# Kernel optimization log

Hardware: AMD Instinct MI355X
Metric: run time of the kernel (lower is better)

The kernel has to match this reference:

```python
import jax, jax.numpy as jnp
import numpy as np

B, C, H, W = 16, 512, 48, 48


def setup_inputs() -> dict:
    key = jax.random.key(0)
    k1, k2 = jax.random.split(key)
    rgb = jax.random.normal(k1, (B, C, H, W), dtype=jnp.float32)
    depth = jax.random.normal(k2, (B, C, H, W), dtype=jnp.float32)
    return {"rgb": rgb, "depth": depth}


def reference(rgb, depth):
    b, c, h, w = rgb.shape
    hw = h * w
    q = rgb.reshape(b, c, hw)              # [B, C, HW]
    k = depth.reshape(b, c, hw)            # [B, C, HW]
    # channel-affinity: energy[b, i, j] = <rgb_chan_i, depth_chan_j>
    energy = jnp.einsum('bcn,bdn->bcd', q, k)   # [B, C, C]
    cl_index = jnp.argmax(energy, axis=2)       # [B, C] best-matching depth channel per rgb channel
    # gather matched depth channels and fuse
    gathered = depth[jnp.arange(b)[:, None], cl_index]  # [B, C, H, W]
    return rgb + gathered
```

## Files before the change

### kernel.cpp

```cpp
#include <hip/hip_runtime.h>
#include <stdint.h>

#define BATCH 16
#define CH    512
#define HW    2304
#define BM    128
#define BN    128
#define BK    32
#define NKT   (HW / BK)

typedef _Float16 half8  __attribute__((ext_vector_type(8)));
typedef float    f32x16 __attribute__((ext_vector_type(16)));

#define AH_OFF 0
#define AL_OFF 8192
#define BH_OFF 16384
#define BL_OFF 24576
#define BUF_SZ 32768

#define MFMA16 __builtin_amdgcn_mfma_f32_32x32x16_f16

__device__ __forceinline__ uint32_t f32_sortable(float f) {
    uint32_t u = __float_as_uint(f);
    return (u & 0x80000000u) ? ~u : (u | 0x80000000u);
}

__device__ __forceinline__ int swz(int r, int cb) {
    return r * 64 + (cb ^ ((r & 3) << 4));
}

__device__ __forceinline__ void cvt8(const float4& v0, const float4& v1,
                                     half8& h, half8& l) {
    float vv[8] = {v0.x, v0.y, v0.z, v0.w, v1.x, v1.y, v1.z, v1.w};
    #pragma unroll
    for (int j = 0; j < 8; ++j) {
        _Float16 hh = (_Float16)vv[j];
        h[j] = hh;
        l[j] = (_Float16)(vv[j] - (float)hh);
    }
}

__device__ __forceinline__ void load_tile(const float* aG, const float* bG, int k0,
                                          float4 (&av)[4], float4 (&bv)[4], int half) {
    av[0] = *(const float4*)(aG + k0 + half * 8 + 0);
    av[1] = *(const float4*)(aG + k0 + half * 8 + 4);
    av[2] = *(const float4*)(aG + k0 + half * 8 + 16);
    av[3] = *(const float4*)(aG + k0 + half * 8 + 20);
    bv[0] = *(const float4*)(bG + k0 + half * 8 + 0);
    bv[1] = *(const float4*)(bG + k0 + half * 8 + 4);
    bv[2] = *(const float4*)(bG + k0 + half * 8 + 16);
    bv[3] = *(const float4*)(bG + k0 + half * 8 + 20);
}

__device__ __forceinline__ void stage_tile(char* dst,
                                           const float4 (&av)[4], const float4 (&bv)[4],
                                           int row, int half) {
    half8 h, l;
    cvt8(av[0], av[1], h, l);
    *(half8*)(dst + AH_OFF + swz(row, half * 16)) = h;
    *(half8*)(dst + AL_OFF + swz(row, half * 16)) = l;
    cvt8(av[2], av[3], h, l);
    *(half8*)(dst + AH_OFF + swz(row, 32 + half * 16)) = h;
    *(half8*)(dst + AL_OFF + swz(row, 32 + half * 16)) = l;
    cvt8(bv[0], bv[1], h, l);
    *(half8*)(dst + BH_OFF + swz(row, half * 16)) = h;
    *(half8*)(dst + BL_OFF + swz(row, half * 16)) = l;
    cvt8(bv[2], bv[3], h, l);
    *(half8*)(dst + BH_OFF + swz(row, 32 + half * 16)) = h;
    *(half8*)(dst + BL_OFF + swz(row, 32 + half * 16)) = l;
}

__device__ __forceinline__ void compute_tile(const char* buf, int rA0, int rB0, int hb,
                                             f32x16& a00, f32x16& a01,
                                             f32x16& a10, f32x16& a11) {
    #pragma unroll
    for (int kc = 0; kc < 2; ++kc) {
        const int cb = kc * 32 + hb;
        half8 ah0 = *(const half8*)(buf + AH_OFF + swz(rA0,      cb));
        half8 ah1 = *(const half8*)(buf + AH_OFF + swz(rA0 + 32, cb));
        half8 al0 = *(const half8*)(buf + AL_OFF + swz(rA0,      cb));
        half8 al1 = *(const half8*)(buf + AL_OFF + swz(rA0 + 32, cb));
        half8 bh0 = *(const half8*)(buf + BH_OFF + swz(rB0,      cb));
        half8 bh1 = *(const half8*)(buf + BH_OFF + swz(rB0 + 32, cb));
        half8 bl0 = *(const half8*)(buf + BL_OFF + swz(rB0,      cb));
        half8 bl1 = *(const half8*)(buf + BL_OFF + swz(rB0 + 32, cb));
        a00 = MFMA16(ah0, bh0, a00, 0, 0, 0);
        a01 = MFMA16(ah0, bh1, a01, 0, 0, 0);
        a10 = MFMA16(ah1, bh0, a10, 0, 0, 0);
        a11 = MFMA16(ah1, bh1, a11, 0, 0, 0);
        a00 = MFMA16(ah0, bl0, a00, 0, 0, 0);
        a01 = MFMA16(ah0, bl1, a01, 0, 0, 0);
        a10 = MFMA16(ah1, bl0, a10, 0, 0, 0);
        a11 = MFMA16(ah1, bl1, a11, 0, 0, 0);
        a00 = MFMA16(al0, bh0, a00, 0, 0, 0);
        a01 = MFMA16(al0, bh1, a01, 0, 0, 0);
        a10 = MFMA16(al1, bh0, a10, 0, 0, 0);
        a11 = MFMA16(al1, bh1, a11, 0, 0, 0);
    }
}

__global__ __launch_bounds__(256, 1)
void energy_argmax_kernel(const float* __restrict__ q,
                          const float* __restrict__ kmat,
                          unsigned long long* __restrict__ best)
{
    const int bid = blockIdx.x;
    const int nid = (bid & 7) * 32 + (bid >> 3);
    const int d0  = (nid & 3) * BN;
    const int c0  = ((nid >> 2) & 3) * BM;
    const int b   = nid >> 4;

    const int tid = threadIdx.x;
    const int lane = tid & 63;
    const int w    = tid >> 6;
    const int wm   = w >> 1;
    const int wn   = w & 1;

    __shared__ __align__(16) char sm[2 * BUF_SZ];
    char* buf0 = sm;
    char* buf1 = sm + BUF_SZ;

    const float* qb = q    + (size_t)b * CH * HW;
    const float* kb = kmat + (size_t)b * CH * HW;

    const int row  = tid >> 1, half = tid & 1;
    const float* aG = qb + (size_t)(c0 + row) * HW;
    const float* bG = kb + (size_t)(d0 + row) * HW;

    float4 av0[4], bv0[4], av1[4], bv1[4];

    load_tile(aG, bG, 0, av0, bv0, half);
    stage_tile(buf0, av0, bv0, row, half);
    load_tile(aG, bG, BK, av1, bv1, half);
    __syncthreads();

    f32x16 a00 = {}, a01 = {}, a10 = {}, a11 = {};

    const int rA0 = wm * 64 + (lane & 31);
    const int rB0 = wn * 64 + (lane & 31);
    const int hb  = (lane >> 5) * 16;

    for (int kt = 0; kt < NKT; kt += 2) {
        if (kt + 2 < NKT) load_tile(aG, bG, (kt + 2) * BK, av0, bv0, half);
        compute_tile(buf0, rA0, rB0, hb, a00, a01, a10, a11);
        stage_tile(buf1, av1, bv1, row, half);
        __syncthreads();
        if (kt + 3 < NKT) load_tile(aG, bG, (kt + 3) * BK, av1, bv1, half);
        compute_tile(buf1, rA0, rB0, hb, a00, a01, a10, a11);
        if (kt + 2 < NKT) stage_tile(buf0, av0, bv0, row, half);
        __syncthreads();
    }

    const uint32_t didx0 = ~(uint32_t)(d0 + wn * 64 +      (lane & 31));
    const uint32_t didx1 = ~(uint32_t)(d0 + wn * 64 + 32 + (lane & 31));
    #pragma unroll
    for (int mi = 0; mi < 2; ++mi) {
        #pragma unroll
        for (int qr = 0; qr < 16; ++qr) {
            float v0 = (mi == 0) ? a00[qr] : a10[qr];
            float v1 = (mi == 0) ? a01[qr] : a11[qr];
            int rowl = wm * 64 + mi * 32 + (qr & 3) + 8 * (qr >> 2) + 4 * (lane >> 5);
            unsigned long long p0 =
                ((unsigned long long)f32_sortable(v0) << 32) | didx0;
            unsigned long long p1 =
                ((unsigned long long)f32_sortable(v1) << 32) | didx1;
            unsigned long long p = p0 > p1 ? p0 : p1;
            #pragma unroll
            for (int off = 1; off < 32; off <<= 1) {
                unsigned long long o = __shfl_xor(p, off, 64);
                if (o > p) p = o;
            }
            if ((lane & 31) == 0)
                atomicMax(&best[(size_t)b * CH + c0 + rowl], p);
        }
    }
}

__global__ __launch_bounds__(256)
void gather_add_kernel(const float* __restrict__ rgb,
                       const float* __restrict__ depth,
                       const unsigned long long* __restrict__ best,
                       float* __restrict__ out)
{
    const int row = blockIdx.x;
    const int b   = row >> 9;
    const uint32_t idx = ~(uint32_t)(best[row] & 0xFFFFFFFFull);
    const float4* src = (const float4*)(rgb   + (size_t)row * HW);
    const float4* dep = (const float4*)(depth + ((size_t)b * CH + idx) * HW);
    float4*       dst = (float4*)(out + (size_t)row * HW);
    for (int j = threadIdx.x; j < HW / 4; j += 256) {
        float4 a = src[j], d = dep[j];
        float4 r; r.x = a.x + d.x; r.y = a.y + d.y; r.z = a.z + d.z; r.w = a.w + d.w;
        dst[j] = r;
    }
}

extern "C" void kernel_launch(void* const* d_in, const int* in_sizes, int n_in,
                              void* d_out, int out_size, void* d_ws, size_t ws_size,
                              hipStream_t stream)
{
    const float* rgb   = (const float*)d_in[0];
    const float* depth = (const float*)d_in[1];
    float* out = (float*)d_out;
    unsigned long long* best = (unsigned long long*)d_ws;

    hipMemsetAsync(best, 0, (size_t)BATCH * CH * sizeof(unsigned long long), stream);

    energy_argmax_kernel<<<256, 256, 0, stream>>>(rgb, depth, best);

    gather_add_kernel<<<BATCH * CH, 256, 0, stream>>>(rgb, depth, best, out);
}
```

Before: 126.9 us.

## Stream fp32 tiles via direct-to-LDS DMA with triple buffering and split-K warps

Replaces the register-staged global loads and per-tile fp16 hi/lo conversion with global_load_lds DMA of raw fp32 tiles into a swizzled, triple-buffered LDS ring. The hi/lo split now happens at fragment read time. Block size doubles to 512 threads so two warp groups each handle half of every K tile, and their partial accumulators are reduced through LDS before the argmax. This aims to remove VGPR staging and conversion work from the load path and overlap memory with MFMA. The cost is redundant conversion per fragment read, more LDS (96KB), and an extra reduction step.

```diff
diff --git a/kernel.cpp b/kernel.cpp
--- a/kernel.cpp
+++ b/kernel.cpp
@@ -12,10 +12,7 @@
 typedef _Float16 half8  __attribute__((ext_vector_type(8)));
 typedef float    f32x16 __attribute__((ext_vector_type(16)));
 
-#define AH_OFF 0
-#define AL_OFF 8192
-#define BH_OFF 16384
-#define BL_OFF 24576
+#define TILE_A 16384
 #define BUF_SZ 32768
 
 #define MFMA16 __builtin_amdgcn_mfma_f32_32x32x16_f16
@@ -25,12 +22,29 @@
     return (u & 0x80000000u) ? ~u : (u | 0x80000000u);
 }
 
-__device__ __forceinline__ int swz(int r, int cb) {
-    return r * 64 + (cb ^ ((r & 3) << 4));
-}
-
-__device__ __forceinline__ void cvt8(const float4& v0, const float4& v1,
-                                     half8& h, half8& l) {
+__device__ __forceinline__ int swzf32(int r, int s) {
+    return r * 128 + ((s ^ (r & 7)) << 4);
+}
+
+__device__ __forceinline__ void dma16(const float* g, char* l) {
+    __builtin_amdgcn_global_load_lds(
+        (const __attribute__((address_space(1))) void*)g,
+        (__attribute__((address_space(3))) void*)l, 16, 0, 0);
+}
+
+__device__ __forceinline__ void dma_step(char* lb, const float* gA0, const float* gA1,
+                                         const float* gB0, const float* gB1,
+                                         int ko, int w2) {
+    dma16(gA0 + ko, lb + w2 * 1024);
+    dma16(gA1 + ko, lb + w2 * 1024 + 1024);
+    dma16(gB0 + ko, lb + TILE_A + w2 * 1024);
+    dma16(gB1 + ko, lb + TILE_A + w2 * 1024 + 1024);
+}
+
+__device__ __forceinline__ void rdfrag(const char* base, int r, int s0,
+                                       half8& h, half8& l) {
+    float4 v0 = *(const float4*)(base + swzf32(r, s0));
+    float4 v1 = *(const float4*)(base + swzf32(r, s0 + 1));
     float vv[8] = {v0.x, v0.y, v0.z, v0.w, v1.x, v1.y, v1.z, v1.w};
     #pragma unroll
     for (int j = 0; j < 8; ++j) {
@@ -40,66 +54,46 @@
     }
 }
 
-__device__ __forceinline__ void load_tile(const float* aG, const float* bG, int k0,
-                                          float4 (&av)[4], float4 (&bv)[4], int half) {
-    av[0] = *(const float4*)(aG + k0 + half * 8 + 0);
-    av[1] = *(const float4*)(aG + k0 + half * 8 + 4);
-    av[2] = *(const float4*)(aG + k0 + half * 8 + 16);
-    av[3] = *(const float4*)(aG + k0 + half * 8 + 20);
-    bv[0] = *(const float4*)(bG + k0 + half * 8 + 0);
-    bv[1] = *(const float4*)(bG + k0 + half * 8 + 4);
-    bv[2] = *(const float4*)(bG + k0 + half * 8 + 16);
-    bv[3] = *(const float4*)(bG + k0 + half * 8 + 20);
-}
-
-__device__ __forceinline__ void stage_tile(char* dst,
-                                           const float4 (&av)[4], const float4 (&bv)[4],
-                                           int row, int half) {
-    half8 h, l;
-    cvt8(av[0], av[1], h, l);
-    *(half8*)(dst + AH_OFF + swz(row, half * 16)) = h;
-    *(half8*)(dst + AL_OFF + swz(row, half * 16)) = l;
-    cvt8(av[2], av[3], h, l);
-    *(half8*)(dst + AH_OFF + swz(row, 32 + half * 16)) = h;
-    *(half8*)(dst + AL_OFF + swz(row, 32 + half * 16)) = l;
-    cvt8(bv[0], bv[1], h, l);
-    *(half8*)(dst + BH_OFF + swz(row, half * 16)) = h;
-    *(half8*)(dst + BL_OFF + swz(row, half * 16)) = l;
-    cvt8(bv[2], bv[3], h, l);
-    *(half8*)(dst + BH_OFF + swz(row, 32 + half * 16)) = h;
-    *(half8*)(dst + BL_OFF + swz(row, 32 + half * 16)) = l;
-}
-
-__device__ __forceinline__ void compute_tile(const char* buf, int rA0, int rB0, int hb,
+__device__ __forceinline__ void compute_step(const char* buf, int rA0, int rB0, int s0,
                                              f32x16& a00, f32x16& a01,
                                              f32x16& a10, f32x16& a11) {
-    #pragma unroll
-    for (int kc = 0; kc < 2; ++kc) {
-        const int cb = kc * 32 + hb;
-        half8 ah0 = *(const half8*)(buf + AH_OFF + swz(rA0,      cb));
-        half8 ah1 = *(const half8*)(buf + AH_OFF + swz(rA0 + 32, cb));
-        half8 al0 = *(const half8*)(buf + AL_OFF + swz(rA0,      cb));
-        half8 al1 = *(const half8*)(buf + AL_OFF + swz(rA0 + 32, cb));
-        half8 bh0 = *(const half8*)(buf + BH_OFF + swz(rB0,      cb));
-        half8 bh1 = *(const half8*)(buf + BH_OFF + swz(rB0 + 32, cb));
-        half8 bl0 = *(const half8*)(buf + BL_OFF + swz(rB0,      cb));
-        half8 bl1 = *(const half8*)(buf + BL_OFF + swz(rB0 + 32, cb));
-        a00 = MFMA16(ah0, bh0, a00, 0, 0, 0);
-        a01 = MFMA16(ah0, bh1, a01, 0, 0, 0);
-        a10 = MFMA16(ah1, bh0, a10, 0, 0, 0);
-        a11 = MFMA16(ah1, bh1, a11, 0, 0, 0);
-        a00 = MFMA16(ah0, bl0, a00, 0, 0, 0);
-        a01 = MFMA16(ah0, bl1, a01, 0, 0, 0);
-        a10 = MFMA16(ah1, bl0, a10, 0, 0, 0);
-        a11 = MFMA16(ah1, bl1, a11, 0, 0, 0);
-        a00 = MFMA16(al0, bh0, a00, 0, 0, 0);
-        a01 = MFMA16(al0, bh1, a01, 0, 0, 0);
-        a10 = MFMA16(al1, bh0, a10, 0, 0, 0);
-        a11 = MFMA16(al1, bh1, a11, 0, 0, 0);
-    }
-}
-
-__global__ __launch_bounds__(256, 1)
+    const char* bA = buf;
+    const char* bB = buf + TILE_A;
+    half8 ah0, al0, ah1, al1, bh0, bl0, bh1, bl1;
+    rdfrag(bA, rA0,      s0, ah0, al0);
+    rdfrag(bA, rA0 + 32, s0, ah1, al1);
+    rdfrag(bB, rB0,      s0, bh0, bl0);
+    rdfrag(bB, rB0 + 32, s0, bh1, bl1);
+    a00 = MFMA16(ah0, bh0, a00, 0, 0, 0);
+    a01 = MFMA16(ah0, bh1, a01, 0, 0, 0);
+    a10 = MFMA16(ah1, bh0, a10, 0, 0, 0);
+    a11 = MFMA16(ah1, bh1, a11, 0, 0, 0);
+    a00 = MFMA16(ah0, bl0, a00, 0, 0, 0);
+    a01 = MFMA16(ah0, bl1, a01, 0, 0, 0);
+    a10 = MFMA16(ah1, bl0, a10, 0, 0, 0);
+    a11 = MFMA16(ah1, bl1, a11, 0, 0, 0);
+    a00 = MFMA16(al0, bh0, a00, 0, 0, 0);
+    a01 = MFMA16(al0, bh1, a01, 0, 0, 0);
+    a10 = MFMA16(al1, bh0, a10, 0, 0, 0);
+    a11 = MFMA16(al1, bh1, a11, 0, 0, 0);
+}
+
+#define STACC(A, aidx) { \
+    char* bp = sm + (p * 4 + (aidx)) * 4096 + lane * 64; \
+    *(float4*)(bp + ((0 ^ (lane & 3)) << 4)) = make_float4(A[0], A[1], A[2], A[3]); \
+    *(float4*)(bp + ((1 ^ (lane & 3)) << 4)) = make_float4(A[4], A[5], A[6], A[7]); \
+    *(float4*)(bp + ((2 ^ (lane & 3)) << 4)) = make_float4(A[8], A[9], A[10], A[11]); \
+    *(float4*)(bp + ((3 ^ (lane & 3)) << 4)) = make_float4(A[12], A[13], A[14], A[15]); }
+
+#define LDACC(A, aidx) { \
+    const char* bp = sm + (p * 4 + (aidx)) * 4096 + lane * 64; \
+    float4 v; \
+    v = *(const float4*)(bp + ((0 ^ (lane & 3)) << 4)); A[0]+=v.x; A[1]+=v.y; A[2]+=v.z; A[3]+=v.w; \
+    v = *(const float4*)(bp + ((1 ^ (lane & 3)) << 4)); A[4]+=v.x; A[5]+=v.y; A[6]+=v.z; A[7]+=v.w; \
+    v = *(const float4*)(bp + ((2 ^ (lane & 3)) << 4)); A[8]+=v.x; A[9]+=v.y; A[10]+=v.z; A[11]+=v.w; \
+    v = *(const float4*)(bp + ((3 ^ (lane & 3)) << 4)); A[12]+=v.x; A[13]+=v.y; A[14]+=v.z; A[15]+=v.w; }
+
+__global__ __launch_bounds__(512, 2)
 void energy_argmax_kernel(const float* __restrict__ q,
                           const float* __restrict__ kmat,
                           unsigned long long* __restrict__ best)
@@ -110,68 +104,76 @@
     const int c0  = ((nid >> 2) & 3) * BM;
     const int b   = nid >> 4;
 
-    const int tid = threadIdx.x;
+    const int tid  = threadIdx.x;
     const int lane = tid & 63;
     const int w    = tid >> 6;
-    const int wm   = w >> 1;
-    const int wn   = w & 1;
-
-    __shared__ __align__(16) char sm[2 * BUF_SZ];
-    char* buf0 = sm;
-    char* buf1 = sm + BUF_SZ;
+    const int kc   = w >> 2;
+    const int p    = w & 3;
+    const int wm   = p >> 1, wn = p & 1;
+    const int w2   = 2 * w;
+
+    __shared__ __align__(16) char sm[3 * BUF_SZ];
 
     const float* qb = q    + (size_t)b * CH * HW;
     const float* kb = kmat + (size_t)b * CH * HW;
 
-    const int row  = tid >> 1, half = tid & 1;
-    const float* aG = qb + (size_t)(c0 + row) * HW;
-    const float* bG = kb + (size_t)(d0 + row) * HW;
-
-    float4 av0[4], bv0[4], av1[4], bv1[4];
-
-    load_tile(aG, bG, 0, av0, bv0, half);
-    stage_tile(buf0, av0, bv0, row, half);
-    load_tile(aG, bG, BK, av1, bv1, half);
-    __syncthreads();
+    const int dml = (lane >> 3) * HW + (((lane & 7) ^ (lane >> 3)) << 2);
+    const float* gA0 = qb + (size_t)(c0 + 16 * w)     * HW + dml;
+    const float* gA1 = qb + (size_t)(c0 + 16 * w + 8) * HW + dml;
+    const float* gB0 = kb + (size_t)(d0 + 16 * w)     * HW + dml;
+    const float* gB1 = kb + (size_t)(d0 + 16 * w + 8) * HW + dml;
+
+    dma_step(sm,          gA0, gA1, gB0, gB1, 0,  w2);
+    dma_step(sm + BUF_SZ, gA0, gA1, gB0, gB1, BK, w2);
+    asm volatile("s_waitcnt vmcnt(4)" ::: "memory");
+    __builtin_amdgcn_s_barrier();
+    __builtin_amdgcn_sched_barrier(0);
 
     f32x16 a00 = {}, a01 = {}, a10 = {}, a11 = {};
-
     const int rA0 = wm * 64 + (lane & 31);
     const int rB0 = wn * 64 + (lane & 31);
-    const int hb  = (lane >> 5) * 16;
-
-    for (int kt = 0; kt < NKT; kt += 2) {
-        if (kt + 2 < NKT) load_tile(aG, bG, (kt + 2) * BK, av0, bv0, half);
-        compute_tile(buf0, rA0, rB0, hb, a00, a01, a10, a11);
-        stage_tile(buf1, av1, bv1, row, half);
-        __syncthreads();
-        if (kt + 3 < NKT) load_tile(aG, bG, (kt + 3) * BK, av1, bv1, half);
-        compute_tile(buf1, rA0, rB0, hb, a00, a01, a10, a11);
-        if (kt + 2 < NKT) stage_tile(buf0, av0, bv0, row, half);
-        __syncthreads();
-    }
-
-    const uint32_t didx0 = ~(uint32_t)(d0 + wn * 64 +      (lane & 31));
-    const uint32_t didx1 = ~(uint32_t)(d0 + wn * 64 + 32 + (lane & 31));
-    #pragma unroll
-    for (int mi = 0; mi < 2; ++mi) {
+    const int s0  = 4 * kc + 2 * (lane >> 5);
+
+    for (int t = 0; t < NKT - 2; ++t) {
+        dma_step(sm + ((t + 2) % 3) * BUF_SZ, gA0, gA1, gB0, gB1, (t + 2) * BK, w2);
+        compute_step(sm + (t % 3) * BUF_SZ, rA0, rB0, s0, a00, a01, a10, a11);
+        asm volatile("s_waitcnt vmcnt(4)" ::: "memory");
+        __builtin_amdgcn_s_barrier();
+        __builtin_amdgcn_sched_barrier(0);
+    }
+    compute_step(sm + ((NKT - 2) % 3) * BUF_SZ, rA0, rB0, s0, a00, a01, a10, a11);
+    asm volatile("s_waitcnt vmcnt(0)" ::: "memory");
+    __builtin_amdgcn_s_barrier();
+    __builtin_amdgcn_sched_barrier(0);
+    compute_step(sm + ((NKT - 1) % 3) * BUF_SZ, rA0, rB0, s0, a00, a01, a10, a11);
+
+    if (w >= 4) { STACC(a00, 0) STACC(a01, 1) STACC(a10, 2) STACC(a11, 3) }
+    __syncthreads();
+    if (w < 4) {
+        LDACC(a00, 0) LDACC(a01, 1) LDACC(a10, 2) LDACC(a11, 3)
+
+        const uint32_t didx0 = ~(uint32_t)(d0 + wn * 64 +      (lane & 31));
+        const uint32_t didx1 = ~(uint32_t)(d0 + wn * 64 + 32 + (lane & 31));
         #pragma unroll
-        for (int qr = 0; qr < 16; ++qr) {
-            float v0 = (mi == 0) ? a00[qr] : a10[qr];
-            float v1 = (mi == 0) ? a01[qr] : a11[qr];
-            int rowl = wm * 64 + mi * 32 + (qr & 3) + 8 * (qr >> 2) + 4 * (lane >> 5);
-            unsigned long long p0 =
-                ((unsigned long long)f32_sortable(v0) << 32) | didx0;
-            unsigned long long p1 =
-                ((unsigned long long)f32_sortable(v1) << 32) | didx1;
-            unsigned long long p = p0 > p1 ? p0 : p1;
+        for (int mi = 0; mi < 2; ++mi) {
             #pragma unroll
-            for (int off = 1; off < 32; off <<= 1) {
-                unsigned long long o = __shfl_xor(p, off, 64);
-                if (o > p) p = o;
+            for (int qr = 0; qr < 16; ++qr) {
+                float v0 = (mi == 0) ? a00[qr] : a10[qr];
+                float v1 = (mi == 0) ? a01[qr] : a11[qr];
+                int rowl = wm * 64 + mi * 32 + (qr & 3) + 8 * (qr >> 2) + 4 * (lane >> 5);
+                unsigned long long p0 =
+                    ((unsigned long long)f32_sortable(v0) << 32) | didx0;
+                unsigned long long p1 =
+                    ((unsigned long long)f32_sortable(v1) << 32) | didx1;
+                unsigned long long pk = p0 > p1 ? p0 : p1;
+                #pragma unroll
+                for (int off = 1; off < 32; off <<= 1) {
+                    unsigned long long o = __shfl_xor(pk, off, 64);
+                    if (o > pk) pk = o;
+                }
+                if ((lane & 31) == 0)
+                    atomicMax(&best[(size_t)b * CH + c0 + rowl], pk);
             }
-            if ((lane & 31) == 0)
-                atomicMax(&best[(size_t)b * CH + c0 + rowl], p);
         }
     }
 }
@@ -206,7 +208,7 @@
 
     hipMemsetAsync(best, 0, (size_t)BATCH * CH * sizeof(unsigned long long), stream);
 
-    energy_argmax_kernel<<<256, 256, 0, stream>>>(rgb, depth, best);
+    energy_argmax_kernel<<<256, 512, 0, stream>>>(rgb, depth, best);
 
     gather_add_kernel<<<BATCH * CH, 256, 0, stream>>>(rgb, depth, best, out);
 }
```

New measurement: 133.0 us. 1.05x slower.
